# Performance work log

Hardware: AMD Instinct MI355X
Metric: run time of the kernel (lower is better)

The kernel has to match this reference:

```python
import jax, jax.numpy as jnp
import numpy as np

HIDDEN = 1024
B, LQ, LK = 8, 2048, 2048


def setup_inputs() -> dict:
    key = jax.random.key(0)
    k1, k2, k3 = jax.random.split(key, 3)
    query = jax.random.normal(k1, (B, LQ, HIDDEN), dtype=jnp.float32)
    key_t = jax.random.normal(k2, (B, LK, HIDDEN), dtype=jnp.float32)
    # multiplicative binary mask on scores (float 0/1)
    attention_mask = jax.random.randint(k3, (B, LQ, LK), 0, 2).astype(jnp.float32)
    return {"query": query, "key": key_t, "attention_mask": attention_mask}


def reference(query, key, attention_mask):
    sqrt_dim = np.sqrt(HIDDEN).astype(np.float32)
    # [B, Lq, Lk] scores, scaled then multiplicatively masked (NOT additive)
    score = jnp.einsum("bqd,bkd->bqk", query, key) / sqrt_dim
    score = score * attention_mask
    attn = jax.nn.softmax(score, axis=-1)
    # NOTE: original module multiplies attn by KEY (not value)
    context = jnp.einsum("bqk,bkd->bqd", attn, key)
    return (context, attn)
```

## Files before the change

kernel.cpp:

```cpp
#include <hip/hip_runtime.h>
#include <hip/hip_bf16.h>


typedef __attribute__((ext_vector_type(8))) short bf16x8;
typedef __attribute__((ext_vector_type(4))) float f32x4;
typedef __attribute__((ext_vector_type(4))) unsigned u32x4;
typedef __attribute__((ext_vector_type(2))) unsigned u32x2;

constexpr int BATCH = 8;
constexpr int LQ    = 2048;
constexpr int LKK   = 2048;
constexpr int DH    = 1024;
constexpr float SCALE = 0.03125f;

constexpr int BM = 128, BN = 128, TK = 32;

#define GAS(p) ((const __attribute__((address_space(1))) void*)(p))
#define LAS(p) ((__attribute__((address_space(3))) void*)(p))

__device__ __forceinline__ unsigned pack_bf16x2(float x0, float x1) {
    unsigned a = __builtin_bit_cast(unsigned, x0) + 0x8000u;
    unsigned b = __builtin_bit_cast(unsigned, x1) + 0x8000u;
    return __builtin_amdgcn_perm(b, a, 0x07060302u);
}

__global__ __launch_bounds__(256)
void cvt_kernel(const float* __restrict__ Q, const float* __restrict__ K,
                unsigned short* __restrict__ Qb, unsigned short* __restrict__ Kb) {
    const int bid = blockIdx.x;
    const float* src; unsigned short* dst; size_t off;
    if (bid < 4096) { src = Q; dst = Qb; off = (size_t)bid * 4096; }
    else            { src = K; dst = Kb; off = (size_t)(bid - 4096) * 4096; }
    off += (size_t)threadIdx.x * 16;
    const f32x4 a = *(const f32x4*)(src + off);
    const f32x4 b = *(const f32x4*)(src + off + 4);
    const f32x4 c = *(const f32x4*)(src + off + 8);
    const f32x4 d = *(const f32x4*)(src + off + 12);
    u32x4 v0, v1;
    v0[0] = pack_bf16x2(a[0], a[1]); v0[1] = pack_bf16x2(a[2], a[3]);
    v0[2] = pack_bf16x2(b[0], b[1]); v0[3] = pack_bf16x2(b[2], b[3]);
    v1[0] = pack_bf16x2(c[0], c[1]); v1[1] = pack_bf16x2(c[2], c[3]);
    v1[2] = pack_bf16x2(d[0], d[1]); v1[3] = pack_bf16x2(d[2], d[3]);
    *(u32x4*)(dst + off)     = v0;
    *(u32x4*)(dst + off + 8) = v1;
}

__global__ __launch_bounds__(256)
void kt_kernel(const float* __restrict__ K, unsigned short* __restrict__ KT) {
    const int b  = blockIdx.z;
    const int k0 = blockIdx.y * 64;
    const int d0 = blockIdx.x * 64;
    const int t  = threadIdx.x;
    const int k4 = (t >> 4) * 4;
    const int d4 = (t & 15) * 4;
    f32x4 rk[4];
    const float* Kp = K + ((size_t)b * LKK + k0 + k4) * DH + d0 + d4;
#pragma unroll
    for (int j = 0; j < 4; ++j) rk[j] = *(const f32x4*)(Kp + (size_t)j * DH);
    unsigned short* Tp = KT + ((size_t)b * DH + d0 + d4) * LKK + k0 + k4;
#pragma unroll
    for (int c = 0; c < 4; ++c) {
        u32x2 w;
        w[0] = pack_bf16x2(rk[0][c], rk[1][c]);
        w[1] = pack_bf16x2(rk[2][c], rk[3][c]);
        *(u32x2*)(Tp + (size_t)c * LKK) = w;
    }
}

__global__ __launch_bounds__(256)
void qk_fast(const unsigned short* __restrict__ Qb, const unsigned short* __restrict__ Kb,
             const float* __restrict__ M, float* __restrict__ S) {
    __shared__ unsigned short lA[BM * TK];
    __shared__ unsigned short lB[BN * TK];

    const int b  = blockIdx.z;
    const int q0 = blockIdx.y * BM;
    const int n0 = blockIdx.x * BN;
    const unsigned short* Ab = Qb + ((size_t)b * LQ  + q0) * DH;
    const unsigned short* Bb = Kb + ((size_t)b * LKK + n0) * DH;

    const int tid  = threadIdx.x;
    const int lane = tid & 63;
    const int wid  = tid >> 6;
    const int wm   = (wid & 1) * 64;
    const int wn   = (wid >> 1) * 64;
    const int lrow = lane & 15;
    const int quad = lane >> 4;
    const int l4   = lane >> 2;
    const int lb   = lane & 3;

    f32x4 acc[4][4];
#pragma unroll
    for (int i = 0; i < 4; ++i)
#pragma unroll
        for (int j = 0; j < 4; ++j) acc[i][j] = (f32x4){0.f, 0.f, 0.f, 0.f};

    for (int k0 = 0; k0 < DH; k0 += TK) {
        __syncthreads();
#pragma unroll
        for (int n = 0; n < 2; ++n) {
            const int row = wid * 32 + n * 16 + l4;
            __builtin_amdgcn_global_load_lds(GAS(Ab + (size_t)row * DH + k0 + lb * 8),
                                             LAS(&lA[(wid * 2 + n) * 512]), 16, 0, 0);
            __builtin_amdgcn_global_load_lds(GAS(Bb + (size_t)row * DH + k0 + lb * 8),
                                             LAS(&lB[(wid * 2 + n) * 512]), 16, 0, 0);
        }
        __syncthreads();

        bf16x8 af[4], bfr[4];
#pragma unroll
        for (int i = 0; i < 4; ++i) {
            af[i]  = *(const bf16x8*)&lA[(wm + i * 16 + lrow) * TK + quad * 8];
            bfr[i] = *(const bf16x8*)&lB[(wn + i * 16 + lrow) * TK + quad * 8];
        }
#pragma unroll
        for (int i = 0; i < 4; ++i)
#pragma unroll
            for (int j = 0; j < 4; ++j)
                acc[i][j] = __builtin_amdgcn_mfma_f32_16x16x32_bf16(af[i], bfr[j], acc[i][j], 0, 0, 0);
    }

    const size_t base = (size_t)b * LQ * LKK;
#pragma unroll
    for (int i = 0; i < 4; ++i) {
#pragma unroll
        for (int r = 0; r < 4; ++r) {
            const int row = q0 + wm + i * 16 + quad * 4 + r;
            const size_t rbase = base + (size_t)row * LKK;
#pragma unroll
            for (int j = 0; j < 4; ++j) {
                const int col = n0 + wn + j * 16 + lrow;
                S[rbase + col] = acc[i][j][r] * SCALE * M[rbase + col];
            }
        }
    }
}

__global__ __launch_bounds__(256)
void softmax_kernel(float* __restrict__ A, unsigned short* __restrict__ ab) {
    float* p = A + (size_t)blockIdx.x * LKK;
    const int tid  = threadIdx.x;
    const int lane = tid & 63;
    const int wid  = tid >> 6;

    f32x4 v0 = *(const f32x4*)(p + tid * 8);
    f32x4 v1 = *(const f32x4*)(p + tid * 8 + 4);

    float m = v0[0];
#pragma unroll
    for (int i = 1; i < 4; ++i) m = fmaxf(m, v0[i]);
#pragma unroll
    for (int i = 0; i < 4; ++i) m = fmaxf(m, v1[i]);
#pragma unroll
    for (int o = 32; o >= 1; o >>= 1) m = fmaxf(m, __shfl_xor(m, o, 64));

    __shared__ float red[8];
    if (lane == 0) red[wid] = m;
    __syncthreads();
    m = fmaxf(fmaxf(red[0], red[1]), fmaxf(red[2], red[3]));

    float s = 0.f;
    f32x4 e0, e1;
#pragma unroll
    for (int i = 0; i < 4; ++i) { e0[i] = __expf(v0[i] - m); s += e0[i]; }
#pragma unroll
    for (int i = 0; i < 4; ++i) { e1[i] = __expf(v1[i] - m); s += e1[i]; }
#pragma unroll
    for (int o = 32; o >= 1; o >>= 1) s += __shfl_xor(s, o, 64);
    if (lane == 0) red[4 + wid] = s;
    __syncthreads();
    const float inv = 1.f / (red[4] + red[5] + red[6] + red[7]);

#pragma unroll
    for (int i = 0; i < 4; ++i) { e0[i] *= inv; e1[i] *= inv; }
    *(f32x4*)(p + tid * 8)     = e0;
    *(f32x4*)(p + tid * 8 + 4) = e1;

    if (ab) {
        u32x4 w;
        w[0] = pack_bf16x2(e0[0], e0[1]); w[1] = pack_bf16x2(e0[2], e0[3]);
        w[2] = pack_bf16x2(e1[0], e1[1]); w[3] = pack_bf16x2(e1[2], e1[3]);
        *(u32x4*)(ab + (size_t)blockIdx.x * LKK + tid * 8) = w;
    }
}

__global__ __launch_bounds__(256)
void pk_fast(const unsigned short* __restrict__ Pb, const unsigned short* __restrict__ KT,
             float* __restrict__ C) {
    __shared__ unsigned short lA[BM * TK];
    __shared__ unsigned short lB[BN * TK];

    const int b  = blockIdx.z;
    const int q0 = blockIdx.y * BM;
    const int n0 = blockIdx.x * BN;
    const unsigned short* Ab = Pb + ((size_t)b * LQ + q0) * LKK;
    const unsigned short* Bb = KT + ((size_t)b * DH + n0) * LKK;

    const int tid  = threadIdx.x;
    const int lane = tid & 63;
    const int wid  = tid >> 6;
    const int wm   = (wid & 1) * 64;
    const int wn   = (wid >> 1) * 64;
    const int lrow = lane & 15;
    const int quad = lane >> 4;
    const int l4   = lane >> 2;
    const int lb   = lane & 3;

    f32x4 acc[4][4];
#pragma unroll
    for (int i = 0; i < 4; ++i)
#pragma unroll
        for (int j = 0; j < 4; ++j) acc[i][j] = (f32x4){0.f, 0.f, 0.f, 0.f};

    for (int k0 = 0; k0 < LKK; k0 += TK) {
        __syncthreads();
#pragma unroll
        for (int n = 0; n < 2; ++n) {
            const int row = wid * 32 + n * 16 + l4;
            __builtin_amdgcn_global_load_lds(GAS(Ab + (size_t)row * LKK + k0 + lb * 8),
                                             LAS(&lA[(wid * 2 + n) * 512]), 16, 0, 0);
            __builtin_amdgcn_global_load_lds(GAS(Bb + (size_t)row * LKK + k0 + lb * 8),
                                             LAS(&lB[(wid * 2 + n) * 512]), 16, 0, 0);
        }
        __syncthreads();

        bf16x8 af[4], bfr[4];
#pragma unroll
        for (int i = 0; i < 4; ++i) {
            af[i]  = *(const bf16x8*)&lA[(wm + i * 16 + lrow) * TK + quad * 8];
            bfr[i] = *(const bf16x8*)&lB[(wn + i * 16 + lrow) * TK + quad * 8];
        }
#pragma unroll
        for (int i = 0; i < 4; ++i)
#pragma unroll
            for (int j = 0; j < 4; ++j)
                acc[i][j] = __builtin_amdgcn_mfma_f32_16x16x32_bf16(af[i], bfr[j], acc[i][j], 0, 0, 0);
    }

    const size_t cb = (size_t)b * LQ * DH;
#pragma unroll
    for (int i = 0; i < 4; ++i) {
#pragma unroll
        for (int r = 0; r < 4; ++r) {
            const int row = q0 + wm + i * 16 + quad * 4 + r;
            const size_t rbase = cb + (size_t)row * DH;
#pragma unroll
            for (int j = 0; j < 4; ++j)
                C[rbase + n0 + wn + j * 16 + lrow] = acc[i][j][r];
        }
    }
}

constexpr int LDSS = 40;
__global__ __launch_bounds__(256, 2)
void pk_kernel(const float* __restrict__ P, const float* __restrict__ K,
               float* __restrict__ C) {
    __shared__ unsigned short lA[BM * LDSS];
    __shared__ unsigned short lB[BN * LDSS];

    const int b  = blockIdx.z;
    const int q0 = blockIdx.y * BM;
    const int n0 = blockIdx.x * BN;
    const float* Pp = P + (size_t)b * LQ * LKK + (size_t)q0 * LKK;
    const float* Kb = K + (size_t)b * LKK * DH;

    const int tid  = threadIdx.x;
    const int lane = tid & 63;
    const int wid  = tid >> 6;
    const int wm   = (wid & 1) * 64;
    const int wn   = (wid >> 1) * 64;
    const int lrow = lane & 15;
    const int quad = lane >> 4;

    f32x4 acc[4][4];
#pragma unroll
    for (int i = 0; i < 4; ++i)
#pragma unroll
        for (int j = 0; j < 4; ++j) acc[i][j] = (f32x4){0.f, 0.f, 0.f, 0.f};

    const int srow = tid >> 3;
    const int skq  = (tid & 7) << 2;
    const int tdb  = tid >> 3;
    const int tkb  = tid & 7;

    for (int k0 = 0; k0 < LKK; k0 += TK) {
        __syncthreads();
#pragma unroll
        for (int i = 0; i < 4; ++i) {
            const int row = i * 32 + srow;
            const f32x4 va = *(const f32x4*)(Pp + (size_t)row * LKK + k0 + skq);
            unsigned* pa = (unsigned*)&lA[row * LDSS + skq];
            pa[0] = pack_bf16x2(va[0], va[1]);
            pa[1] = pack_bf16x2(va[2], va[3]);
        }
        f32x4 rk[4];
#pragma unroll
        for (int j = 0; j < 4; ++j)
            rk[j] = *(const f32x4*)(Kb + (size_t)(k0 + tkb * 4 + j) * DH + n0 + tdb * 4);
#pragma unroll
        for (int c = 0; c < 4; ++c) {
            unsigned* pb = (unsigned*)&lB[(tdb * 4 + c) * LDSS + tkb * 4];
            pb[0] = pack_bf16x2(rk[0][c], rk[1][c]);
            pb[1] = pack_bf16x2(rk[2][c], rk[3][c]);
        }
        __syncthreads();

        bf16x8 af[4], bfr[4];
#pragma unroll
        for (int i = 0; i < 4; ++i) {
            af[i]  = *(const bf16x8*)&lA[(wm + i * 16 + lrow) * LDSS + quad * 8];
            bfr[i] = *(const bf16x8*)&lB[(wn + i * 16 + lrow) * LDSS + quad * 8];
        }
#pragma unroll
        for (int i = 0; i < 4; ++i)
#pragma unroll
            for (int j = 0; j < 4; ++j)
                acc[i][j] = __builtin_amdgcn_mfma_f32_16x16x32_bf16(af[i], bfr[j], acc[i][j], 0, 0, 0);
    }

    const size_t cb = (size_t)b * LQ * DH;
#pragma unroll
    for (int i = 0; i < 4; ++i) {
#pragma unroll
        for (int r = 0; r < 4; ++r) {
            const int row = q0 + wm + i * 16 + quad * 4 + r;
            const size_t rbase = cb + (size_t)row * DH;
#pragma unroll
            for (int j = 0; j < 4; ++j)
                C[rbase + n0 + wn + j * 16 + lrow] = acc[i][j][r];
        }
    }
}

extern "C" void kernel_launch(void* const* d_in, const int* in_sizes, int n_in,
                              void* d_out, int out_size, void* d_ws, size_t ws_size,
                              hipStream_t stream) {
    const float* Q = (const float*)d_in[0];
    const float* K = (const float*)d_in[1];
    const float* M = (const float*)d_in[2];

    constexpr size_t QEL  = (size_t)BATCH * LQ * DH;
    constexpr size_t AEL  = (size_t)BATCH * LQ * LKK;
    constexpr size_t KTEL = (size_t)BATCH * DH * LKK;

    float* ctx  = (float*)d_out;
    float* attn = ctx + QEL;

    unsigned short* Qb = (unsigned short*)ctx;
    unsigned short* Kb = Qb + QEL;

    const bool wsOK = ws_size >= (KTEL + AEL) * sizeof(unsigned short);
    unsigned short* KT = (unsigned short*)d_ws;
    unsigned short* ab = KT + KTEL;

    cvt_kernel<<<dim3(8192), 256, 0, stream>>>(Q, K, Qb, Kb);
    if (wsOK)
        kt_kernel<<<dim3(DH / 64, LKK / 64, BATCH), 256, 0, stream>>>(K, KT);
    qk_fast<<<dim3(LKK / BN, LQ / BM, BATCH), 256, 0, stream>>>(Qb, Kb, M, attn);
    softmax_kernel<<<dim3(BATCH * LQ), 256, 0, stream>>>(attn, wsOK ? ab : nullptr);
    if (wsOK)
        pk_fast<<<dim3(DH / BN, LQ / BM, BATCH), 256, 0, stream>>>(ab, KT, ctx);
    else
        pk_kernel<<<dim3(DH / BN, LQ / BM, BATCH), 256, 0, stream>>>(attn, K, ctx);
}
```

Before: 660.7 us.

## Replace QK and PK GEMMs with 256x256 pipelined, swizzled 8-wave kernels

Both bf16 GEMMs now share one mainloop with 256x256 tiles, 512 threads and a 64-wide K step. It multi-buffers global-to-LDS loads six stages ahead with explicit vmcnt waits, XOR-swizzles the LDS layout to avoid bank conflicts, and raises wave priority around the MFMA bursts. Block indices are remapped so neighbouring blocks share operands in L2. This aims to cut LDS stalls, sync overhead and global traffic per flop, at the cost of 128KB of LDS per block, heavy register use and fragile hand-tuned waitcnt logic.

```diff
diff --git a/kernel.cpp b/kernel.cpp
--- a/kernel.cpp
+++ b/kernel.cpp
@@ -12,8 +12,6 @@
 constexpr int LKK   = 2048;
 constexpr int DH    = 1024;
 constexpr float SCALE = 0.03125f;
-
-constexpr int BM = 128, BN = 128, TK = 32;
 
 #define GAS(p) ((const __attribute__((address_space(1))) void*)(p))
 #define LAS(p) ((__attribute__((address_space(3))) void*)(p))
@@ -67,17 +65,231 @@
     }
 }
 
+template<int LDA, int LDB, int NT>
+__device__ __forceinline__ void gemm8_mainloop(
+    const unsigned short* __restrict__ Ab,
+    const unsigned short* __restrict__ Bb,
+    unsigned short* lA, unsigned short* lB,
+    f32x4 (&acc)[8][4])
+{
+    const int tid  = threadIdx.x;
+    const int lane = tid & 63;
+    const int wid  = tid >> 6;
+    const int wm   = (wid & 1) * 128;
+    const int wn   = (wid >> 1) * 64;
+    const int lrow = lane & 15;
+    const int quad = lane >> 4;
+    const int slotsw = (quad ^ ((lrow >> 1) & 3)) * 8;
+
+    const int srow0 = wid * 32 + (lane >> 2);
+    const int srow1 = srow0 + 16;
+    const int sc    = ((lane & 3) ^ ((lane >> 3) & 3)) * 8;
+
+    auto stage = [&](int I) {
+        const int tile = I >> 2;
+        const int h    = I & 3;
+        const int kh   = h >> 1;
+        const int kb   = tile * 64 + kh * 32 + sc;
+        const unsigned short* s = (h & 1) ? Bb : Ab;
+        const int ld            = (h & 1) ? LDB : LDA;
+        unsigned short* d = ((h & 1) ? lB : lA)
+                          + (tile & 1) * 16384 + kh * 8192 + wid * 1024;
+        __builtin_amdgcn_global_load_lds(GAS(s + (size_t)srow0 * ld + kb), LAS(d),       16, 0, 0);
+        __builtin_amdgcn_global_load_lds(GAS(s + (size_t)srow1 * ld + kb), LAS(d + 512), 16, 0, 0);
+    };
+
+#pragma unroll
+    for (int i = 0; i < 8; ++i)
+#pragma unroll
+        for (int j = 0; j < 4; ++j) acc[i][j] = (f32x4){0.f, 0.f, 0.f, 0.f};
+
+#pragma unroll
+    for (int I = 0; I < 6; ++I) stage(I);
+    asm volatile("s_waitcnt vmcnt(4)" ::: "memory");
+    __builtin_amdgcn_s_barrier();
+
+    for (int T = 0; T < NT; ++T) {
+        const int par = (T & 1) * 16384;
+        bf16x8 bfr[4];
+#pragma unroll
+        for (int q = 0; q < 4; ++q) {
+            const int kh = (q >> 1) * 8192;
+            const int mh = (q & 1) * 4;
+            if ((q & 1) == 0) {
+#pragma unroll
+                for (int nf = 0; nf < 4; ++nf)
+                    bfr[nf] = *(const bf16x8*)&lB[par + kh + (wn + nf * 16 + lrow) * 32 + slotsw];
+            }
+            bf16x8 af[4];
+#pragma unroll
+            for (int mf = 0; mf < 4; ++mf)
+                af[mf] = *(const bf16x8*)&lA[par + kh + (wm + (mh + mf) * 16 + lrow) * 32 + slotsw];
+
+            if (4 * T + q + 6 < 4 * NT) stage(4 * T + q + 6);
+
+            __builtin_amdgcn_s_barrier();
+            __builtin_amdgcn_s_setprio(1);
+#pragma unroll
+            for (int mf = 0; mf < 4; ++mf)
+#pragma unroll
+                for (int nf = 0; nf < 4; ++nf)
+                    acc[mh + mf][nf] = __builtin_amdgcn_mfma_f32_16x16x32_bf16(
+                        af[mf], bfr[nf], acc[mh + mf][nf], 0, 0, 0);
+            __builtin_amdgcn_s_setprio(0);
+            if (q == 3) {
+                if (T < NT - 2)       asm volatile("s_waitcnt vmcnt(4)" ::: "memory");
+                else if (T == NT - 2) asm volatile("s_waitcnt vmcnt(0)" ::: "memory");
+            }
+            __builtin_amdgcn_s_barrier();
+        }
+    }
+}
+
+__global__ __launch_bounds__(512, 2)
+void qk8(const unsigned short* __restrict__ Qb, const unsigned short* __restrict__ Kb,
+         const float* __restrict__ M, float* __restrict__ S) {
+    __shared__ __align__(16) unsigned short lA[32768];
+    __shared__ __align__(16) unsigned short lB[32768];
+
+    const int l   = blockIdx.x;
+    const int swz = (l & 7) * 64 + (l >> 3);
+    const int b   = swz >> 6;
+    const int my  = (swz >> 3) & 7;
+    const int nx  = swz & 7;
+    const int q0  = my * 256;
+    const int n0  = nx * 256;
+
+    const unsigned short* Ap = Qb + ((size_t)b * LQ  + q0) * DH;
+    const unsigned short* Bp = Kb + ((size_t)b * LKK + n0) * DH;
+
+    f32x4 acc[8][4];
+    gemm8_mainloop<DH, DH, DH / 64>(Ap, Bp, lA, lB, acc);
+
+    const int lane = threadIdx.x & 63;
+    const int wid  = threadIdx.x >> 6;
+    const int wm   = (wid & 1) * 128;
+    const int wn   = (wid >> 1) * 64;
+    const int lrow = lane & 15;
+    const int quad = lane >> 4;
+
+    const size_t base = (size_t)b * LQ * LKK;
+#pragma unroll
+    for (int mf = 0; mf < 8; ++mf) {
+#pragma unroll
+        for (int r = 0; r < 4; ++r) {
+            const int row = q0 + wm + mf * 16 + quad * 4 + r;
+            const size_t rb = base + (size_t)row * LKK;
+#pragma unroll
+            for (int nf = 0; nf < 4; ++nf) {
+                const int col = n0 + wn + nf * 16 + lrow;
+                S[rb + col] = acc[mf][nf][r] * SCALE * M[rb + col];
+            }
+        }
+    }
+}
+
 __global__ __launch_bounds__(256)
-void qk_fast(const unsigned short* __restrict__ Qb, const unsigned short* __restrict__ Kb,
-             const float* __restrict__ M, float* __restrict__ S) {
-    __shared__ unsigned short lA[BM * TK];
-    __shared__ unsigned short lB[BN * TK];
+void softmax_kernel(float* __restrict__ A, unsigned short* __restrict__ ab) {
+    float* p = A + (size_t)blockIdx.x * LKK;
+    const int tid  = threadIdx.x;
+    const int lane = tid & 63;
+    const int wid  = tid >> 6;
+
+    f32x4 v0 = *(const f32x4*)(p + tid * 8);
+    f32x4 v1 = *(const f32x4*)(p + tid * 8 + 4);
+
+    float m = v0[0];
+#pragma unroll
+    for (int i = 1; i < 4; ++i) m = fmaxf(m, v0[i]);
+#pragma unroll
+    for (int i = 0; i < 4; ++i) m = fmaxf(m, v1[i]);
+#pragma unroll
+    for (int o = 32; o >= 1; o >>= 1) m = fmaxf(m, __shfl_xor(m, o, 64));
+
+    __shared__ float red[8];
+    if (lane == 0) red[wid] = m;
+    __syncthreads();
+    m = fmaxf(fmaxf(red[0], red[1]), fmaxf(red[2], red[3]));
+
+    float s = 0.f;
+    f32x4 e0, e1;
+#pragma unroll
+    for (int i = 0; i < 4; ++i) { e0[i] = __expf(v0[i] - m); s += e0[i]; }
+#pragma unroll
+    for (int i = 0; i < 4; ++i) { e1[i] = __expf(v1[i] - m); s += e1[i]; }
+#pragma unroll
+    for (int o = 32; o >= 1; o >>= 1) s += __shfl_xor(s, o, 64);
+    if (lane == 0) red[4 + wid] = s;
+    __syncthreads();
+    const float inv = 1.f / (red[4] + red[5] + red[6] + red[7]);
+
+#pragma unroll
+    for (int i = 0; i < 4; ++i) { e0[i] *= inv; e1[i] *= inv; }
+    *(f32x4*)(p + tid * 8)     = e0;
+    *(f32x4*)(p + tid * 8 + 4) = e1;
+
+    if (ab) {
+        u32x4 w;
+        w[0] = pack_bf16x2(e0[0], e0[1]); w[1] = pack_bf16x2(e0[2], e0[3]);
+        w[2] = pack_bf16x2(e1[0], e1[1]); w[3] = pack_bf16x2(e1[2], e1[3]);
+        *(u32x4*)(ab + (size_t)blockIdx.x * LKK + tid * 8) = w;
+    }
+}
+
+__global__ __launch_bounds__(512, 2)
+void pk8(const unsigned short* __restrict__ Pb, const unsigned short* __restrict__ KT,
+         float* __restrict__ C) {
+    __shared__ __align__(16) unsigned short lA[32768];
+    __shared__ __align__(16) unsigned short lB[32768];
+
+    const int l   = blockIdx.x;
+    const int swz = (l & 7) * 32 + (l >> 3);
+    const int b   = swz >> 5;
+    const int my  = (swz >> 2) & 7;
+    const int nx  = swz & 3;
+    const int q0  = my * 256;
+    const int n0  = nx * 256;
+
+    const unsigned short* Ap = Pb + ((size_t)b * LQ + q0) * LKK;
+    const unsigned short* Bp = KT + ((size_t)b * DH + n0) * LKK;
+
+    f32x4 acc[8][4];
+    gemm8_mainloop<LKK, LKK, LKK / 64>(Ap, Bp, lA, lB, acc);
+
+    const int lane = threadIdx.x & 63;
+    const int wid  = threadIdx.x >> 6;
+    const int wm   = (wid & 1) * 128;
+    const int wn   = (wid >> 1) * 64;
+    const int lrow = lane & 15;
+    const int quad = lane >> 4;
+
+    const size_t cb = (size_t)b * LQ * DH;
+#pragma unroll
+    for (int mf = 0; mf < 8; ++mf) {
+#pragma unroll
+        for (int r = 0; r < 4; ++r) {
+            const int row = q0 + wm + mf * 16 + quad * 4 + r;
+            const size_t rbase = cb + (size_t)row * DH;
+#pragma unroll
+            for (int nf = 0; nf < 4; ++nf)
+                C[rbase + n0 + wn + nf * 16 + lrow] = acc[mf][nf][r];
+        }
+    }
+}
+
+constexpr int BM = 128, BN = 128, TK = 32;
+constexpr int LDSS = 40;
+__global__ __launch_bounds__(256, 2)
+void pk_kernel(const float* __restrict__ P, const float* __restrict__ K,
+               float* __restrict__ C) {
+    __shared__ unsigned short lA[BM * LDSS];
+    __shared__ unsigned short lB[BN * LDSS];
 
     const int b  = blockIdx.z;
     const int q0 = blockIdx.y * BM;
     const int n0 = blockIdx.x * BN;
-    const unsigned short* Ab = Qb + ((size_t)b * LQ  + q0) * DH;
-    const unsigned short* Bb = Kb + ((size_t)b * LKK + n0) * DH;
+    const float* Pp = P + (size_t)b * LQ * LKK + (size_t)q0 * LKK;
+    const float* Kb = K + (size_t)b * LKK * DH;
 
     const int tid  = threadIdx.x;
     const int lane = tid & 63;
@@ -86,191 +298,6 @@
     const int wn   = (wid >> 1) * 64;
     const int lrow = lane & 15;
     const int quad = lane >> 4;
-    const int l4   = lane >> 2;
-    const int lb   = lane & 3;
-
-    f32x4 acc[4][4];
-#pragma unroll
-    for (int i = 0; i < 4; ++i)
-#pragma unroll
-        for (int j = 0; j < 4; ++j) acc[i][j] = (f32x4){0.f, 0.f, 0.f, 0.f};
-
-    for (int k0 = 0; k0 < DH; k0 += TK) {
-        __syncthreads();
-#pragma unroll
-        for (int n = 0; n < 2; ++n) {
-            const int row = wid * 32 + n * 16 + l4;
-            __builtin_amdgcn_global_load_lds(GAS(Ab + (size_t)row * DH + k0 + lb * 8),
-                                             LAS(&lA[(wid * 2 + n) * 512]), 16, 0, 0);
-            __builtin_amdgcn_global_load_lds(GAS(Bb + (size_t)row * DH + k0 + lb * 8),
-                                             LAS(&lB[(wid * 2 + n) * 512]), 16, 0, 0);
-        }
-        __syncthreads();
-
-        bf16x8 af[4], bfr[4];
-#pragma unroll
-        for (int i = 0; i < 4; ++i) {
-            af[i]  = *(const bf16x8*)&lA[(wm + i * 16 + lrow) * TK + quad * 8];
-            bfr[i] = *(const bf16x8*)&lB[(wn + i * 16 + lrow) * TK + quad * 8];
-        }
-#pragma unroll
-        for (int i = 0; i < 4; ++i)
-#pragma unroll
-            for (int j = 0; j < 4; ++j)
-                acc[i][j] = __builtin_amdgcn_mfma_f32_16x16x32_bf16(af[i], bfr[j], acc[i][j], 0, 0, 0);
-    }
-
-    const size_t base = (size_t)b * LQ * LKK;
-#pragma unroll
-    for (int i = 0; i < 4; ++i) {
-#pragma unroll
-        for (int r = 0; r < 4; ++r) {
-            const int row = q0 + wm + i * 16 + quad * 4 + r;
-            const size_t rbase = base + (size_t)row * LKK;
-#pragma unroll
-            for (int j = 0; j < 4; ++j) {
-                const int col = n0 + wn + j * 16 + lrow;
-                S[rbase + col] = acc[i][j][r] * SCALE * M[rbase + col];
-            }
-        }
-    }
-}
-
-__global__ __launch_bounds__(256)
-void softmax_kernel(float* __restrict__ A, unsigned short* __restrict__ ab) {
-    float* p = A + (size_t)blockIdx.x * LKK;
-    const int tid  = threadIdx.x;
-    const int lane = tid & 63;
-    const int wid  = tid >> 6;
-
-    f32x4 v0 = *(const f32x4*)(p + tid * 8);
-    f32x4 v1 = *(const f32x4*)(p + tid * 8 + 4);
-
-    float m = v0[0];
-#pragma unroll
-    for (int i = 1; i < 4; ++i) m = fmaxf(m, v0[i]);
-#pragma unroll
-    for (int i = 0; i < 4; ++i) m = fmaxf(m, v1[i]);
-#pragma unroll
-    for (int o = 32; o >= 1; o >>= 1) m = fmaxf(m, __shfl_xor(m, o, 64));
-
-    __shared__ float red[8];
-    if (lane == 0) red[wid] = m;
-    __syncthreads();
-    m = fmaxf(fmaxf(red[0], red[1]), fmaxf(red[2], red[3]));
-
-    float s = 0.f;
-    f32x4 e0, e1;
-#pragma unroll
-    for (int i = 0; i < 4; ++i) { e0[i] = __expf(v0[i] - m); s += e0[i]; }
-#pragma unroll
-    for (int i = 0; i < 4; ++i) { e1[i] = __expf(v1[i] - m); s += e1[i]; }
-#pragma unroll
-    for (int o = 32; o >= 1; o >>= 1) s += __shfl_xor(s, o, 64);
-    if (lane == 0) red[4 + wid] = s;
-    __syncthreads();
-    const float inv = 1.f / (red[4] + red[5] + red[6] + red[7]);
-
-#pragma unroll
-    for (int i = 0; i < 4; ++i) { e0[i] *= inv; e1[i] *= inv; }
-    *(f32x4*)(p + tid * 8)     = e0;
-    *(f32x4*)(p + tid * 8 + 4) = e1;
-
-    if (ab) {
-        u32x4 w;
-        w[0] = pack_bf16x2(e0[0], e0[1]); w[1] = pack_bf16x2(e0[2], e0[3]);
-        w[2] = pack_bf16x2(e1[0], e1[1]); w[3] = pack_bf16x2(e1[2], e1[3]);
-        *(u32x4*)(ab + (size_t)blockIdx.x * LKK + tid * 8) = w;
-    }
-}
-
-__global__ __launch_bounds__(256)
-void pk_fast(const unsigned short* __restrict__ Pb, const unsigned short* __restrict__ KT,
-             float* __restrict__ C) {
-    __shared__ unsigned short lA[BM * TK];
-    __shared__ unsigned short lB[BN * TK];
-
-    const int b  = blockIdx.z;
-    const int q0 = blockIdx.y * BM;
-    const int n0 = blockIdx.x * BN;
-    const unsigned short* Ab = Pb + ((size_t)b * LQ + q0) * LKK;
-    const unsigned short* Bb = KT + ((size_t)b * DH + n0) * LKK;
-
-    const int tid  = threadIdx.x;
-    const int lane = tid & 63;
-    const int wid  = tid >> 6;
-    const int wm   = (wid & 1) * 64;
-    const int wn   = (wid >> 1) * 64;
-    const int lrow = lane & 15;
-    const int quad = lane >> 4;
-    const int l4   = lane >> 2;
-    const int lb   = lane & 3;
-
-    f32x4 acc[4][4];
-#pragma unroll
-    for (int i = 0; i < 4; ++i)
-#pragma unroll
-        for (int j = 0; j < 4; ++j) acc[i][j] = (f32x4){0.f, 0.f, 0.f, 0.f};
-
-    for (int k0 = 0; k0 < LKK; k0 += TK) {
-        __syncthreads();
-#pragma unroll
-        for (int n = 0; n < 2; ++n) {
-            const int row = wid * 32 + n * 16 + l4;
-            __builtin_amdgcn_global_load_lds(GAS(Ab + (size_t)row * LKK + k0 + lb * 8),
-                                             LAS(&lA[(wid * 2 + n) * 512]), 16, 0, 0);
-            __builtin_amdgcn_global_load_lds(GAS(Bb + (size_t)row * LKK + k0 + lb * 8),
-                                             LAS(&lB[(wid * 2 + n) * 512]), 16, 0, 0);
-        }
-        __syncthreads();
-
-        bf16x8 af[4], bfr[4];
-#pragma unroll
-        for (int i = 0; i < 4; ++i) {
-            af[i]  = *(const bf16x8*)&lA[(wm + i * 16 + lrow) * TK + quad * 8];
-            bfr[i] = *(const bf16x8*)&lB[(wn + i * 16 + lrow) * TK + quad * 8];
-        }
-#pragma unroll
-        for (int i = 0; i < 4; ++i)
-#pragma unroll
-            for (int j = 0; j < 4; ++j)
-                acc[i][j] = __builtin_amdgcn_mfma_f32_16x16x32_bf16(af[i], bfr[j], acc[i][j], 0, 0, 0);
-    }
-
-    const size_t cb = (size_t)b * LQ * DH;
-#pragma unroll
-    for (int i = 0; i < 4; ++i) {
-#pragma unroll
-        for (int r = 0; r < 4; ++r) {
-            const int row = q0 + wm + i * 16 + quad * 4 + r;
-            const size_t rbase = cb + (size_t)row * DH;
-#pragma unroll
-            for (int j = 0; j < 4; ++j)
-                C[rbase + n0 + wn + j * 16 + lrow] = acc[i][j][r];
-        }
-    }
-}
-
-constexpr int LDSS = 40;
-__global__ __launch_bounds__(256, 2)
-void pk_kernel(const float* __restrict__ P, const float* __restrict__ K,
-               float* __restrict__ C) {
-    __shared__ unsigned short lA[BM * LDSS];
-    __shared__ unsigned short lB[BN * LDSS];
-
-    const int b  = blockIdx.z;
-    const int q0 = blockIdx.y * BM;
-    const int n0 = blockIdx.x * BN;
-    const float* Pp = P + (size_t)b * LQ * LKK + (size_t)q0 * LKK;
-    const float* Kb = K + (size_t)b * LKK * DH;
-
-    const int tid  = threadIdx.x;
-    const int lane = tid & 63;
-    const int wid  = tid >> 6;
-    const int wm   = (wid & 1) * 64;
-    const int wn   = (wid >> 1) * 64;
-    const int lrow = lane & 15;
-    const int quad = lane >> 4;
 
     f32x4 acc[4][4];
 #pragma unroll
@@ -356,10 +383,10 @@
     cvt_kernel<<<dim3(8192), 256, 0, stream>>>(Q, K, Qb, Kb);
     if (wsOK)
         kt_kernel<<<dim3(DH / 64, LKK / 64, BATCH), 256, 0, stream>>>(K, KT);
-    qk_fast<<<dim3(LKK / BN, LQ / BM, BATCH), 256, 0, stream>>>(Qb, Kb, M, attn);
+    qk8<<<dim3(BATCH * (LQ / 256) * (LKK / 256)), 512, 0, stream>>>(Qb, Kb, M, attn);
     softmax_kernel<<<dim3(BATCH * LQ), 256, 0, stream>>>(attn, wsOK ? ab : nullptr);
     if (wsOK)
-        pk_fast<<<dim3(DH / BN, LQ / BM, BATCH), 256, 0, stream>>>(ab, KT, ctx);
+        pk8<<<dim3(BATCH * (LQ / 256) * (DH / 256)), 512, 0, stream>>>(ab, KT, ctx);
     else
         pk_kernel<<<dim3(DH / BN, LQ / BM, BATCH), 256, 0, stream>>>(attn, K, ctx);
 }
```

New measurement: 598.2 us. 9.5% less time.
